# Kernel optimization log

Hardware: AMD Instinct MI355X
Metric: run time of the kernel (lower is better)

The kernel has to match this reference:

```python
import jax, jax.numpy as jnp
import numpy as np

HZ, TAU1, TAU2, TSCALE = 20.0, 0.5, 0.05, 6.0

def _double_exp_kernel(hz, tau1, tau2, tscale):
    # Faithful to SpikeToCalcium.set_double_exp (tau1 > tau2 assumed)
    t1 = tau1 * hz
    t2 = tau2 * hz
    r = t1 / t2
    d = t1 - t2
    scale = np.power(r, -t2 / d) - np.power(r, -t1 / d)
    t = np.arange(1.0, t1 * tscale + 2.0, dtype=np.float32)
    return ((np.exp(-t / t1) - np.exp(-t / t2)) / scale).astype(np.float32)  # size 61

def setup_inputs() -> dict:
    key = jax.random.key(0)
    u = jax.random.uniform(key, (1024, 30000), dtype=jnp.float32)  # [cells, T] spike activity
    kernel = jnp.asarray(_double_exp_kernel(HZ, TAU1, TAU2, TSCALE))  # [K]=61
    return {"u": u, "kernel": kernel}

def reference(u, kernel):
    # Keras: conv1d(u[...,None], kernel[::-1], 'valid'); tf conv = cross-correlation,
    # so with the reversed kernel this is a true causal FIR convolution.
    krev = kernel[::-1]
    out = jax.lax.conv_general_dilated(
        u[:, None, :],              # [N, 1, T]
        krev[None, None, :],        # [O=1, I=1, K]
        window_strides=(1,),
        padding='VALID',
    )  # [N, 1, T-K+1]
    return out[:, 0, :]
```

## Files before the change

kernel.cpp:

```cpp
#include <hip/hip_runtime.h>

#define K_TAPS   61
#define R_OUT    4
#define BLOCK    256
#define TILE_OUT (BLOCK * R_OUT)
#define TILE_IN  (TILE_OUT + K_TAPS - 1)
#define TILE_IN4 ((TILE_IN + 3) / 4)
#define SUBP     272
#define NV       ((R_OUT + K_TAPS - 1) / 4)

__global__ __launch_bounds__(BLOCK)
void SpikeToCalcium_conv1d_kernel(const float* __restrict__ u,
                                  const float* __restrict__ kern,
                                  float* __restrict__ out,
                                  int L, int M, long long total_in)
{
    __shared__ float sx[4 * SUBP];

    const int t          = threadIdx.x;
    const int row        = blockIdx.y;
    const int tile_start = blockIdx.x * TILE_OUT;

    const long long gbase = (long long)row * L + tile_start;
    for (int v = t; v < TILE_IN4; v += BLOCK) {
        const long long g = gbase + 4LL * v;
        float4 val;
        if (g + 3 < total_in) {
            val = *reinterpret_cast<const float4*>(u + g);
        } else {
            val.x = (g + 0 < total_in) ? u[g + 0] : 0.0f;
            val.y = (g + 1 < total_in) ? u[g + 1] : 0.0f;
            val.z = (g + 2 < total_in) ? u[g + 2] : 0.0f;
            val.w = (g + 3 < total_in) ? u[g + 3] : 0.0f;
        }
        sx[0 * SUBP + v] = val.x;
        sx[1 * SUBP + v] = val.y;
        sx[2 * SUBP + v] = val.z;
        sx[3 * SUBP + v] = val.w;
    }
    __syncthreads();

    float acc[R_OUT] = {0.0f, 0.0f, 0.0f, 0.0f};

#pragma unroll
    for (int i = 0; i < NV; ++i) {
#pragma unroll
        for (int j = 0; j < 4; ++j) {
            const float x = sx[j * SUBP + t + i];
            const int p = 4 * i + j;
#pragma unroll
            for (int r = 0; r < R_OUT; ++r) {
                const int k = p - r;
                if (k >= 0 && k < K_TAPS)
                    acc[r] = fmaf(x, kern[K_TAPS - 1 - k], acc[r]);
            }
        }
    }

    const int obase = tile_start + 4 * t;
    const long long o = (long long)row * M + obase;
    if (obase + R_OUT <= M) {
        *reinterpret_cast<float4*>(out + o) =
            make_float4(acc[0], acc[1], acc[2], acc[3]);
    } else {
#pragma unroll
        for (int r = 0; r < R_OUT; ++r)
            if (obase + r < M) out[o + r] = acc[r];
    }
}

extern "C" void kernel_launch(void* const* d_in, const int* in_sizes, int n_in,
                              void* d_out, int out_size, void* d_ws, size_t ws_size,
                              hipStream_t stream) {
    const float* u    = (const float*)d_in[0];
    const float* kern = (const float*)d_in[1];
    float*       out  = (float*)d_out;

    const long long total_in = (long long)in_sizes[0];
    const int ROWS = (int)((total_in - (long long)out_size) / (K_TAPS - 1));
    const int L    = (int)(total_in / ROWS);
    const int M    = L - K_TAPS + 1;

    const int blocks_per_row = (M + TILE_OUT - 1) / TILE_OUT;
    dim3 grid(blocks_per_row, ROWS);
    SpikeToCalcium_conv1d_kernel<<<grid, BLOCK, 0, stream>>>(
        u, kern, out, L, M, total_in);
}
```

Measured before the change: 225.6 us.

## Compute sixteen outputs per thread with a 16-way strided shared-memory layout

Each thread now produces 16 consecutive outputs instead of 4, and the shared-memory input tile is split into 16 interleaved sub-arrays so each thread reads its sliding window conflict-free. This cuts the shared-memory loads per output and amortizes the 60-sample halo over a larger tile, which lowers the redundant global reads and the number of blocks. In exchange it raises register pressure from the 16 accumulators and the larger unrolled loop, and uses a larger shared tile, which may lower occupancy. The output is written as four float4 stores per thread.

```diff
diff --git a/kernel.cpp b/kernel.cpp
--- a/kernel.cpp
+++ b/kernel.cpp
@@ -1,13 +1,13 @@
 #include <hip/hip_runtime.h>
 
 #define K_TAPS   61
-#define R_OUT    4
+#define R_OUT    16
 #define BLOCK    256
 #define TILE_OUT (BLOCK * R_OUT)
 #define TILE_IN  (TILE_OUT + K_TAPS - 1)
-#define TILE_IN4 ((TILE_IN + 3) / 4)
-#define SUBP     272
-#define NV       ((R_OUT + K_TAPS - 1) / 4)
+#define TILE_IN4 (TILE_IN / 4)
+#define SUBP     261
+#define WINP     (R_OUT + K_TAPS - 1)
 
 __global__ __launch_bounds__(BLOCK)
 void SpikeToCalcium_conv1d_kernel(const float* __restrict__ u,
@@ -15,7 +15,7 @@
                                   float* __restrict__ out,
                                   int L, int M, long long total_in)
 {
-    __shared__ float sx[4 * SUBP];
+    __shared__ float sx[16 * SUBP];
 
     const int t          = threadIdx.x;
     const int row        = blockIdx.y;
@@ -33,21 +33,25 @@
             val.z = (g + 2 < total_in) ? u[g + 2] : 0.0f;
             val.w = (g + 3 < total_in) ? u[g + 3] : 0.0f;
         }
-        sx[0 * SUBP + v] = val.x;
-        sx[1 * SUBP + v] = val.y;
-        sx[2 * SUBP + v] = val.z;
-        sx[3 * SUBP + v] = val.w;
+        const int q0 = 4 * v;
+        sx[((q0 + 0) & 15) * SUBP + ((q0 + 0) >> 4)] = val.x;
+        sx[((q0 + 1) & 15) * SUBP + ((q0 + 1) >> 4)] = val.y;
+        sx[((q0 + 2) & 15) * SUBP + ((q0 + 2) >> 4)] = val.z;
+        sx[((q0 + 3) & 15) * SUBP + ((q0 + 3) >> 4)] = val.w;
     }
     __syncthreads();
 
-    float acc[R_OUT] = {0.0f, 0.0f, 0.0f, 0.0f};
+    float acc[R_OUT];
+#pragma unroll
+    for (int r = 0; r < R_OUT; ++r) acc[r] = 0.0f;
 
 #pragma unroll
-    for (int i = 0; i < NV; ++i) {
+    for (int i = 0; i < 5; ++i) {
 #pragma unroll
-        for (int j = 0; j < 4; ++j) {
-            const float x = sx[j * SUBP + t + i];
-            const int p = 4 * i + j;
+        for (int m = 0; m < 16; ++m) {
+            const int p = 16 * i + m;
+            if (p >= WINP) break;
+            const float x = sx[m * SUBP + t + i];
 #pragma unroll
             for (int r = 0; r < R_OUT; ++r) {
                 const int k = p - r;
@@ -57,15 +61,20 @@
         }
     }
 
-    const int obase = tile_start + 4 * t;
+    const int obase = tile_start + R_OUT * t;
     const long long o = (long long)row * M + obase;
-    if (obase + R_OUT <= M) {
-        *reinterpret_cast<float4*>(out + o) =
-            make_float4(acc[0], acc[1], acc[2], acc[3]);
-    } else {
 #pragma unroll
-        for (int r = 0; r < R_OUT; ++r)
-            if (obase + r < M) out[o + r] = acc[r];
+    for (int gI = 0; gI < R_OUT / 4; ++gI) {
+        const int ob = obase + 4 * gI;
+        if (ob + 4 <= M) {
+            *reinterpret_cast<float4*>(out + o + 4 * gI) =
+                make_float4(acc[4 * gI + 0], acc[4 * gI + 1],
+                            acc[4 * gI + 2], acc[4 * gI + 3]);
+        } else {
+#pragma unroll
+            for (int r = 0; r < 4; ++r)
+                if (ob + r < M) out[o + 4 * gI + r] = acc[4 * gI + r];
+        }
     }
 }
 
```

New measurement: 299.2 us. 1.33x slower.
